# Kernel optimization log

Hardware: AMD Instinct MI355X
Metric: run time of the kernel (lower is better)

Reference implementation:

```python
import jax, jax.numpy as jnp
import numpy as np

N_SUB, N_AGR, N_URB = 100000, 200000, 100000
E_SS, E_AS, E_US = 1_600_000, 400_000, 200_000
D_SUB, D_HRU, H, OUT, L = 128, 32, 128, 16, 3


def setup_inputs() -> dict:
    key = jax.random.key(0)
    ks = jax.random.split(key, 20)
    s = 0.05
    inp = {
        "x_sub": jax.random.normal(ks[0], (N_SUB, D_SUB), jnp.float32),
        "x_agr": jax.random.normal(ks[1], (N_AGR, D_HRU), jnp.float32),
        "x_urb": jax.random.normal(ks[2], (N_URB, D_HRU), jnp.float32),
        "ss_src": jax.random.randint(ks[3], (E_SS,), 0, N_SUB, jnp.int32),
        "ss_dst": jax.random.randint(ks[4], (E_SS,), 0, N_SUB, jnp.int32),
        "as_src": jax.random.randint(ks[5], (E_AS,), 0, N_AGR, jnp.int32),
        "as_dst": jax.random.randint(ks[6], (E_AS,), 0, N_SUB, jnp.int32),
        "us_src": jax.random.randint(ks[7], (E_US,), 0, N_URB, jnp.int32),
        "us_dst": jax.random.randint(ks[8], (E_US,), 0, N_SUB, jnp.int32),
        # Stacked per-layer SAGEConv params (in_sub == hidden, so uniform shapes).
        # lin_l (neighbor path, has bias) and lin_r (root path, no bias).
        "Wl_ss": jax.random.normal(ks[9], (L, H, H), jnp.float32) * s,
        "bl_ss": jnp.zeros((L, H), jnp.float32),
        "Wr_ss": jax.random.normal(ks[10], (L, H, H), jnp.float32) * s,
        "Wl_as": jax.random.normal(ks[11], (L, D_HRU, H), jnp.float32) * s,
        "bl_as": jnp.zeros((L, H), jnp.float32),
        "Wr_as": jax.random.normal(ks[12], (L, H, H), jnp.float32) * s,
        "Wl_us": jax.random.normal(ks[13], (L, D_HRU, H), jnp.float32) * s,
        "bl_us": jnp.zeros((L, H), jnp.float32),
        "Wr_us": jax.random.normal(ks[14], (L, H, H), jnp.float32) * s,
        "Wf": jax.random.normal(ks[15], (H, OUT), jnp.float32) * s,
        "bf": jnp.zeros((OUT,), jnp.float32),
    }
    return inp


def reference(x_sub, x_agr, x_urb, ss_src, ss_dst, as_src, as_dst, us_src,
              us_dst, Wl_ss, bl_ss, Wr_ss, Wl_as, bl_as, Wr_as, Wl_us, bl_us,
              Wr_us, Wf, bf):
    # Degree of each sub node under sub->sub edges (for mean aggr, layers>0).
    deg = jax.ops.segment_sum(jnp.ones((E_SS,), x_sub.dtype), ss_dst,
                              num_segments=N_SUB)
    deg = jnp.maximum(deg, 1.0)[:, None]  # [N_SUB,1]

    h = x_sub
    for i in range(L):
        # sub -> sub: gather + scatter-add (sum at layer 0, mean afterwards)
        agg_ss = jax.ops.segment_sum(h[ss_src], ss_dst, num_segments=N_SUB)
        if i > 0:
            agg_ss = agg_ss / deg  # PyG default aggr='mean' for layers > 0
        # hru_agr -> sub and hru_urb -> sub: sum aggregation (sage_aggr='sum')
        agg_as = jax.ops.segment_sum(x_agr[as_src], as_dst, num_segments=N_SUB)
        agg_us = jax.ops.segment_sum(x_urb[us_src], us_dst, num_segments=N_SUB)
        # SAGEConv: lin_l(aggr msgs) + lin_r(x_dst); HeteroConv aggr='sum'.
        out = (agg_ss @ Wl_ss[i] + bl_ss[i] + h @ Wr_ss[i]
               + agg_as @ Wl_as[i] + bl_as[i] + h @ Wr_as[i]
               + agg_us @ Wl_us[i] + bl_us[i] + h @ Wr_us[i])
        h = jax.nn.relu(out)  # norms are Identity; dropout in eval mode
    logits = h @ Wf + bf
    return jax.nn.softmax(logits, axis=1)
```

## Files before the change

kernel.cpp:

```cpp
#include <hip/hip_runtime.h>
#include <hip/hip_bf16.h>

#define N_SUB 100000
#define N_AGR 200000
#define N_URB 100000
#define E_SS  1600000
#define E_AS  400000
#define E_US  200000
#define HID   128
#define DHRU  32
#define NOUT  16
#define NL    3
#define SCAN_T 12500

typedef unsigned short u16;
typedef unsigned int u32;
typedef short bf16x8 __attribute__((ext_vector_type(8)));
typedef float f32x4 __attribute__((ext_vector_type(4)));

static __device__ __forceinline__ u16 f2b(float f) {
    u32 x = __float_as_uint(f);
    u32 r = (x + 0x7fffu + ((x >> 16) & 1u)) >> 16;
    return (u16)r;
}
static __device__ __forceinline__ float blo(u32 u) { return __uint_as_float(u << 16); }
static __device__ __forceinline__ float bhi(u32 u) { return __uint_as_float(u & 0xffff0000u); }


__global__ void hist_kernel(const int* __restrict__ dst, int* __restrict__ deg, int n) {
    int i = blockIdx.x * 256 + threadIdx.x;
    if (i < n) atomicAdd(&deg[dst[i]], 1);
}

__global__ void scan_p1(const int* __restrict__ deg, int* __restrict__ tsum) {
    int i = blockIdx.x * 256 + threadIdx.x;
    if (i >= SCAN_T) return;
    const int4* p = (const int4*)(deg + i * 8);
    int4 a = p[0], b = p[1];
    tsum[i] = a.x + a.y + a.z + a.w + b.x + b.y + b.z + b.w;
}

__global__ void scan_p2(int* __restrict__ tsum) {
    __shared__ int sh[256];
    const int tid = threadIdx.x;
    const int start = tid * 49;
    const int end = min(start + 49, SCAN_T);
    int s = 0;
    for (int i = start; i < end; ++i) s += tsum[i];
    sh[tid] = s;
    __syncthreads();
    for (int o = 1; o < 256; o <<= 1) {
        int t = (tid >= o) ? sh[tid - o] : 0;
        __syncthreads();
        sh[tid] += t;
        __syncthreads();
    }
    int off = (tid > 0) ? sh[tid - 1] : 0;
    for (int i = start; i < end; ++i) {
        int v = tsum[i];
        tsum[i] = off;
        off += v;
    }
}

__global__ void scan_p3(int* __restrict__ degcur, const int* __restrict__ tsum,
                        int* __restrict__ ro, float* __restrict__ inv_deg) {
    int i = blockIdx.x * 256 + threadIdx.x;
    if (i >= SCAN_T) return;
    int off = tsum[i];
#pragma unroll
    for (int j = 0; j < 8; ++j) {
        int idx = i * 8 + j;
        int d = degcur[idx];
        ro[idx] = off;
        inv_deg[idx] = 1.0f / (float)(d > 1 ? d : 1);
        degcur[idx] = off;
        off += d;
    }
    if (i == SCAN_T - 1) ro[N_SUB] = off;
}

__global__ void fill_kernel(const int* __restrict__ src, const int* __restrict__ dst,
                            int* __restrict__ cursor, int* __restrict__ csr, int n) {
    int i = blockIdx.x * 256 + threadIdx.x;
    if (i < n) {
        int p = atomicAdd(&cursor[dst[i]], 1);
        csr[p] = src[i];
    }
}

__global__ void scatter32_kernel(const float* __restrict__ x, const int* __restrict__ src,
                                 const int* __restrict__ dst, float* __restrict__ agg2,
                                 int nE, int off) {
    int t = blockIdx.x * 256 + threadIdx.x;
    int e = t >> 3, j = t & 7;
    if (e >= nE) return;
    int s = src[e], d = dst[e];
    const float4 v = *(const float4*)(x + (size_t)s * 32 + j * 4);
    float* p = agg2 + (size_t)d * 64 + off + j * 4;
    atomicAdd(p + 0, v.x);
    atomicAdd(p + 1, v.y);
    atomicAdd(p + 2, v.z);
    atomicAdd(p + 3, v.w);
}

__global__ void add3_kernel(const float* __restrict__ a, const float* __restrict__ b,
                            const float* __restrict__ c, float* __restrict__ o, int n) {
    int i = blockIdx.x * 256 + threadIdx.x;
    if (i < n) o[i] = a[i] + b[i] + c[i];
}

__global__ void build_bp(const float* __restrict__ Wl_ss, const float* __restrict__ Wr_ss,
                         const float* __restrict__ Wr_as, const float* __restrict__ Wr_us,
                         const float* __restrict__ Wl_as, const float* __restrict__ Wl_us,
                         u16* __restrict__ Bp) {
    int b = blockIdx.x;
    int lane = threadIdx.x;
    int lay = b / 80, rem = b % 80, s = rem / 8, c = rem % 8;
    int col = c * 16 + (lane & 15);
    u16* o = Bp + (size_t)(((lay * 80) + s * 8 + c) * 64 + lane) * 8;
#pragma unroll
    for (int j = 0; j < 8; ++j) {
        int k = s * 32 + (lane >> 4) * 8 + j;
        float v;
        if (k < 128) {
            v = Wl_ss[((size_t)lay * 128 + k) * 128 + col];
        } else if (k < 256) {
            size_t idx = ((size_t)lay * 128 + (k - 128)) * 128 + col;
            v = Wr_ss[idx] + Wr_as[idx] + Wr_us[idx];
        } else if (k < 288) {
            v = Wl_as[((size_t)lay * 32 + (k - 256)) * 128 + col];
        } else {
            v = Wl_us[((size_t)lay * 32 + (k - 288)) * 128 + col];
        }
        o[j] = f2b(v);
    }
}

__global__ void cvt_f32_bf16(const float* __restrict__ in, u16* __restrict__ o, int n4) {
    int i = blockIdx.x * 256 + threadIdx.x;
    if (i >= n4) return;
    float4 v = ((const float4*)in)[i];
    ushort4 u;
    u.x = f2b(v.x); u.y = f2b(v.y); u.z = f2b(v.z); u.w = f2b(v.w);
    ((ushort4*)o)[i] = u;
}

__global__ __launch_bounds__(256)
void agg_ss_bf16(const u32* __restrict__ h32, const int* __restrict__ ro,
                 const int* __restrict__ csr, const float* __restrict__ inv_deg,
                 u32* __restrict__ out32, int n, int use_mean) {
    int node = blockIdx.x * 4 + (threadIdx.x >> 6);
    int lane = threadIdx.x & 63;
    if (node >= n) return;
    int beg = ro[node], end = ro[node + 1];
    float a0 = 0.f, a1 = 0.f;
    int p = beg;
    for (; p + 1 < end; p += 2) {
        int s0 = csr[p], s1 = csr[p + 1];
        u32 u0 = h32[(size_t)s0 * 64 + lane];
        u32 u1 = h32[(size_t)s1 * 64 + lane];
        a0 += blo(u0) + blo(u1);
        a1 += bhi(u0) + bhi(u1);
    }
    if (p < end) {
        u32 u0 = h32[(size_t)csr[p] * 64 + lane];
        a0 += blo(u0);
        a1 += bhi(u0);
    }
    if (use_mean) {
        float iv = inv_deg[node];
        a0 *= iv; a1 *= iv;
    }
    out32[(size_t)node * 64 + lane] = (u32)f2b(a0) | ((u32)f2b(a1) << 16);
}

__global__ __launch_bounds__(256)
void layer_gemm_mfma(const u16* __restrict__ agss, const u16* __restrict__ h,
                     const float* __restrict__ agg2, const u16* __restrict__ Bp,
                     const float* __restrict__ bsum, u16* __restrict__ out, int n) {
    __shared__ __align__(16) u16 tile[4][32][136];
    const int tid = threadIdx.x;
    const int w = tid >> 6, l = tid & 63;
    const int lr = l & 15, lq = l >> 4;
    const int rows0 = blockIdx.x * 128 + w * 32;

    f32x4 acc[2][8];
#pragma unroll
    for (int rf = 0; rf < 2; ++rf)
#pragma unroll
        for (int c = 0; c < 8; ++c) acc[rf][c] = (f32x4){0.f, 0.f, 0.f, 0.f};

    const bf16x8 zf = {0, 0, 0, 0, 0, 0, 0, 0};

#pragma unroll
    for (int s = 0; s < 10; ++s) {
        bf16x8 a[2];
        if (s < 8) {
            const u16* X = (s < 4) ? agss : h;
            int koff = (s & 3) * 32 + lq * 8;
#pragma unroll
            for (int rf = 0; rf < 2; ++rf) {
                int row = rows0 + rf * 16 + lr;
                a[rf] = (row < n) ? *(const bf16x8*)(X + (size_t)row * 128 + koff) : zf;
            }
        } else {
            int koff = (s - 8) * 32 + lq * 8;
#pragma unroll
            for (int rf = 0; rf < 2; ++rf) {
                int row = rows0 + rf * 16 + lr;
                if (row < n) {
                    float4 f0 = *(const float4*)(agg2 + (size_t)row * 64 + koff);
                    float4 f1 = *(const float4*)(agg2 + (size_t)row * 64 + koff + 4);
                    bf16x8 v;
                    v[0] = (short)f2b(f0.x); v[1] = (short)f2b(f0.y);
                    v[2] = (short)f2b(f0.z); v[3] = (short)f2b(f0.w);
                    v[4] = (short)f2b(f1.x); v[5] = (short)f2b(f1.y);
                    v[6] = (short)f2b(f1.z); v[7] = (short)f2b(f1.w);
                    a[rf] = v;
                } else {
                    a[rf] = zf;
                }
            }
        }
        const u16* bp = Bp + ((size_t)(s * 8) * 64 + l) * 8;
#pragma unroll
        for (int c = 0; c < 8; ++c) {
            bf16x8 b = *(const bf16x8*)(bp + (size_t)c * 64 * 8);
            acc[0][c] = __builtin_amdgcn_mfma_f32_16x16x32_bf16(a[0], b, acc[0][c], 0, 0, 0);
            acc[1][c] = __builtin_amdgcn_mfma_f32_16x16x32_bf16(a[1], b, acc[1][c], 0, 0, 0);
        }
    }

    float bias[8];
#pragma unroll
    for (int c = 0; c < 8; ++c) bias[c] = bsum[c * 16 + lr];

#pragma unroll
    for (int rf = 0; rf < 2; ++rf)
#pragma unroll
        for (int c = 0; c < 8; ++c)
#pragma unroll
            for (int r = 0; r < 4; ++r) {
                float v = fmaxf(acc[rf][c][r] + bias[c], 0.f);
                tile[w][rf * 16 + lq * 4 + r][c * 16 + lr] = f2b(v);
            }

#pragma unroll
    for (int i = 0; i < 8; ++i) {
        int row = i * 4 + lq;
        int grow = rows0 + row;
        if (grow < n)
            *(bf16x8*)(out + (size_t)grow * 128 + lr * 8) =
                *(const bf16x8*)&tile[w][row][lr * 8];
    }
}

__global__ __launch_bounds__(256)
void final_kernel(const u32* __restrict__ h32, const float* __restrict__ Wf,
                  const float* __restrict__ bfv, float* __restrict__ out, int n) {
    __shared__ float wsh[HID * NOUT + NOUT];
    for (int i = threadIdx.x; i < HID * NOUT; i += 256) wsh[i] = Wf[i];
    if (threadIdx.x < NOUT) wsh[HID * NOUT + threadIdx.x] = bfv[threadIdx.x];
    __syncthreads();
    int t = blockIdx.x * 256 + threadIdx.x;
    int node = t >> 4, c = t & 15;
    if (node >= n) return;
    const u32* hr = h32 + (size_t)node * 64;
    float acc = wsh[HID * NOUT + c];
#pragma unroll 4
    for (int k2 = 0; k2 < 64; ++k2) {
        u32 u = hr[k2];
        acc += blo(u) * wsh[(2 * k2) * NOUT + c] + bhi(u) * wsh[(2 * k2 + 1) * NOUT + c];
    }
    float m = acc;
#pragma unroll
    for (int o = 8; o >= 1; o >>= 1) m = fmaxf(m, __shfl_xor(m, o, 16));
    float e = expf(acc - m);
    float ssum = e;
#pragma unroll
    for (int o = 8; o >= 1; o >>= 1) ssum += __shfl_xor(ssum, o, 16);
    out[(size_t)node * NOUT + c] = e / ssum;
}

extern "C" void kernel_launch(void* const* d_in, const int* in_sizes, int n_in,
                              void* d_out, int out_size, void* d_ws, size_t ws_size,
                              hipStream_t stream) {
    const float* x_sub = (const float*)d_in[0];
    const float* x_agr = (const float*)d_in[1];
    const float* x_urb = (const float*)d_in[2];
    const int* ss_src = (const int*)d_in[3];
    const int* ss_dst = (const int*)d_in[4];
    const int* as_src = (const int*)d_in[5];
    const int* as_dst = (const int*)d_in[6];
    const int* us_src = (const int*)d_in[7];
    const int* us_dst = (const int*)d_in[8];
    const float* Wl_ss = (const float*)d_in[9];
    const float* bl_ss = (const float*)d_in[10];
    const float* Wr_ss = (const float*)d_in[11];
    const float* Wl_as = (const float*)d_in[12];
    const float* bl_as = (const float*)d_in[13];
    const float* Wr_as = (const float*)d_in[14];
    const float* Wl_us = (const float*)d_in[15];
    const float* bl_us = (const float*)d_in[16];
    const float* Wr_us = (const float*)d_in[17];
    const float* Wf = (const float*)d_in[18];
    const float* bfv = (const float*)d_in[19];
    float* out = (float*)d_out;

    char* ws = (char*)d_ws;
    u16* h0      = (u16*)(ws + 0);
    u16* hA      = (u16*)(ws + 25600000);
    u16* hB      = (u16*)(ws + 51200000);
    u16* agss    = (u16*)(ws + 76800000);
    float* agg2f = (float*)(ws + 102400000);
    float* inv_deg = (float*)(ws + 128000000);
    int* ro      = (int*)(ws + 128400000);
    int* degcur  = (int*)(ws + 128800016);
    int* csr     = (int*)(ws + 129200016);
    int* tsum    = (int*)(ws + 129200016);
    u16* Bp      = (u16*)(ws + 135600016);
    float* b_sum = (float*)(ws + 135845776);

    hipMemsetAsync(degcur, 0, N_SUB * sizeof(int), stream);
    hist_kernel<<<(E_SS + 255) / 256, 256, 0, stream>>>(ss_dst, degcur, E_SS);
    scan_p1<<<(SCAN_T + 255) / 256, 256, 0, stream>>>(degcur, tsum);
    scan_p2<<<1, 256, 0, stream>>>(tsum);
    scan_p3<<<(SCAN_T + 255) / 256, 256, 0, stream>>>(degcur, tsum, ro, inv_deg);
    fill_kernel<<<(E_SS + 255) / 256, 256, 0, stream>>>(ss_src, ss_dst, degcur, csr, E_SS);

    hipMemsetAsync(agg2f, 0, (size_t)N_SUB * 64 * sizeof(float), stream);
    scatter32_kernel<<<(E_AS * 8 + 255) / 256, 256, 0, stream>>>(x_agr, as_src, as_dst, agg2f, E_AS, 0);
    scatter32_kernel<<<(E_US * 8 + 255) / 256, 256, 0, stream>>>(x_urb, us_src, us_dst, agg2f, E_US, 32);

    build_bp<<<240, 64, 0, stream>>>(Wl_ss, Wr_ss, Wr_as, Wr_us, Wl_as, Wl_us, Bp);
    add3_kernel<<<2, 256, 0, stream>>>(bl_ss, bl_as, bl_us, b_sum, NL * HID);

    cvt_f32_bf16<<<(N_SUB * HID / 4 + 255) / 256, 256, 0, stream>>>(x_sub, h0, N_SUB * HID / 4);

    const int agg_grid = (N_SUB + 3) / 4;
    const int gemm_grid = (N_SUB + 127) / 128;
    const size_t BPL = 40960;

    agg_ss_bf16<<<agg_grid, 256, 0, stream>>>((const u32*)h0, ro, csr, inv_deg, (u32*)agss, N_SUB, 0);
    layer_gemm_mfma<<<gemm_grid, 256, 0, stream>>>(agss, h0, agg2f, Bp + 0 * BPL, b_sum + 0 * HID, hA, N_SUB);

    agg_ss_bf16<<<agg_grid, 256, 0, stream>>>((const u32*)hA, ro, csr, inv_deg, (u32*)agss, N_SUB, 1);
    layer_gemm_mfma<<<gemm_grid, 256, 0, stream>>>(agss, hA, agg2f, Bp + 1 * BPL, b_sum + 1 * HID, hB, N_SUB);

    agg_ss_bf16<<<agg_grid, 256, 0, stream>>>((const u32*)hB, ro, csr, inv_deg, (u32*)agss, N_SUB, 1);
    layer_gemm_mfma<<<gemm_grid, 256, 0, stream>>>(agss, hB, agg2f, Bp + 2 * BPL, b_sum + 2 * HID, hA, N_SUB);

    final_kernel<<<(N_SUB * NOUT + 255) / 256, 256, 0, stream>>>((const u32*)hA, Wf, bfv, out, N_SUB);
}
```

Before: 930.4 us.

## Replace atomic HRU scatter with CSR gather and store bf16 aggregates

The agr->sub and urb->sub aggregations no longer scatter with float atomics. The code now builds CSR structures for both edge sets (histogram, scan, fill) and runs a per-node gather kernel that writes the summed result directly as bf16. The GEMM kernel then reads these bf16 aggregates like its other inputs instead of converting fp32 on every layer. This removes 2.4M float atomics, the 25.6MB memset and the per-layer fp32 reads, at the cost of extra histogram, scan and fill launches and atomics on the cursor arrays.

After: 798.4 us. -14.2%, faster.

```diff
diff --git a/kernel.cpp b/kernel.cpp
--- a/kernel.cpp
+++ b/kernel.cpp
@@ -64,7 +64,7 @@
 }
 
 __global__ void scan_p3(int* __restrict__ degcur, const int* __restrict__ tsum,
-                        int* __restrict__ ro, float* __restrict__ inv_deg) {
+                        int* __restrict__ ro, float* inv_deg) {
     int i = blockIdx.x * 256 + threadIdx.x;
     if (i >= SCAN_T) return;
     int off = tsum[i];
@@ -73,7 +73,7 @@
         int idx = i * 8 + j;
         int d = degcur[idx];
         ro[idx] = off;
-        inv_deg[idx] = 1.0f / (float)(d > 1 ? d : 1);
+        if (inv_deg) inv_deg[idx] = 1.0f / (float)(d > 1 ? d : 1);
         degcur[idx] = off;
         off += d;
     }
@@ -89,19 +89,25 @@
     }
 }
 
-__global__ void scatter32_kernel(const float* __restrict__ x, const int* __restrict__ src,
-                                 const int* __restrict__ dst, float* __restrict__ agg2,
-                                 int nE, int off) {
-    int t = blockIdx.x * 256 + threadIdx.x;
-    int e = t >> 3, j = t & 7;
-    if (e >= nE) return;
-    int s = src[e], d = dst[e];
-    const float4 v = *(const float4*)(x + (size_t)s * 32 + j * 4);
-    float* p = agg2 + (size_t)d * 64 + off + j * 4;
-    atomicAdd(p + 0, v.x);
-    atomicAdd(p + 1, v.y);
-    atomicAdd(p + 2, v.z);
-    atomicAdd(p + 3, v.w);
+__global__ __launch_bounds__(256)
+void agg2_gather(const float* __restrict__ x_agr, const float* __restrict__ x_urb,
+                 const int* __restrict__ ro_as, const int* __restrict__ csr_as,
+                 const int* __restrict__ ro_us, const int* __restrict__ csr_us,
+                 u16* __restrict__ agg2b, int n) {
+    int node = blockIdx.x * 4 + (threadIdx.x >> 6);
+    int lane = threadIdx.x & 63;
+    if (node >= n) return;
+    const bool is_us = lane >= 32;
+    const int col = lane & 31;
+    const int* ro = is_us ? ro_us : ro_as;
+    const int* csr = is_us ? csr_us : csr_as;
+    const float* x = is_us ? x_urb : x_agr;
+    int beg = ro[node], end = ro[node + 1];
+    float acc = 0.f;
+    for (int p = beg; p < end; ++p) {
+        acc += x[(size_t)csr[p] * 32 + col];
+    }
+    agg2b[(size_t)node * 64 + lane] = f2b(acc);
 }
 
 __global__ void add3_kernel(const float* __restrict__ a, const float* __restrict__ b,
@@ -177,7 +183,7 @@
 
 __global__ __launch_bounds__(256)
 void layer_gemm_mfma(const u16* __restrict__ agss, const u16* __restrict__ h,
-                     const float* __restrict__ agg2, const u16* __restrict__ Bp,
+                     const u16* __restrict__ agg2b, const u16* __restrict__ Bp,
                      const float* __restrict__ bsum, u16* __restrict__ out, int n) {
     __shared__ __align__(16) u16 tile[4][32][136];
     const int tid = threadIdx.x;
@@ -195,33 +201,16 @@
 
 #pragma unroll
     for (int s = 0; s < 10; ++s) {
+        const u16* X;
+        int ld, koff;
+        if (s < 4)      { X = agss;  ld = 128; koff = s * 32 + lq * 8; }
+        else if (s < 8) { X = h;     ld = 128; koff = (s - 4) * 32 + lq * 8; }
+        else            { X = agg2b; ld = 64;  koff = (s - 8) * 32 + lq * 8; }
         bf16x8 a[2];
-        if (s < 8) {
-            const u16* X = (s < 4) ? agss : h;
-            int koff = (s & 3) * 32 + lq * 8;
-#pragma unroll
-            for (int rf = 0; rf < 2; ++rf) {
-                int row = rows0 + rf * 16 + lr;
-                a[rf] = (row < n) ? *(const bf16x8*)(X + (size_t)row * 128 + koff) : zf;
-            }
-        } else {
-            int koff = (s - 8) * 32 + lq * 8;
-#pragma unroll
-            for (int rf = 0; rf < 2; ++rf) {
-                int row = rows0 + rf * 16 + lr;
-                if (row < n) {
-                    float4 f0 = *(const float4*)(agg2 + (size_t)row * 64 + koff);
-                    float4 f1 = *(const float4*)(agg2 + (size_t)row * 64 + koff + 4);
-                    bf16x8 v;
-                    v[0] = (short)f2b(f0.x); v[1] = (short)f2b(f0.y);
-                    v[2] = (short)f2b(f0.z); v[3] = (short)f2b(f0.w);
-                    v[4] = (short)f2b(f1.x); v[5] = (short)f2b(f1.y);
-                    v[6] = (short)f2b(f1.z); v[7] = (short)f2b(f1.w);
-                    a[rf] = v;
-                } else {
-                    a[rf] = zf;
-                }
-            }
+#pragma unroll
+        for (int rf = 0; rf < 2; ++rf) {
+            int row = rows0 + rf * 16 + lr;
+            a[rf] = (row < n) ? *(const bf16x8*)(X + (size_t)row * ld + koff) : zf;
         }
         const u16* bp = Bp + ((size_t)(s * 8) * 64 + l) * 8;
 #pragma unroll
@@ -313,25 +302,43 @@
     u16* hA      = (u16*)(ws + 25600000);
     u16* hB      = (u16*)(ws + 51200000);
     u16* agss    = (u16*)(ws + 76800000);
-    float* agg2f = (float*)(ws + 102400000);
-    float* inv_deg = (float*)(ws + 128000000);
-    int* ro      = (int*)(ws + 128400000);
-    int* degcur  = (int*)(ws + 128800016);
-    int* csr     = (int*)(ws + 129200016);
-    int* tsum    = (int*)(ws + 129200016);
-    u16* Bp      = (u16*)(ws + 135600016);
-    float* b_sum = (float*)(ws + 135845776);
-
-    hipMemsetAsync(degcur, 0, N_SUB * sizeof(int), stream);
-    hist_kernel<<<(E_SS + 255) / 256, 256, 0, stream>>>(ss_dst, degcur, E_SS);
-    scan_p1<<<(SCAN_T + 255) / 256, 256, 0, stream>>>(degcur, tsum);
+    u16* agg2b   = (u16*)(ws + 102400000);
+    float* inv_deg = (float*)(ws + 115200000);
+    int* ro_ss   = (int*)(ws + 115600000);
+    int* ro_as   = (int*)(ws + 116000016);
+    int* ro_us   = (int*)(ws + 116400032);
+    int* deg_ss  = (int*)(ws + 116800048);
+    int* deg_as  = (int*)(ws + 117200048);
+    int* deg_us  = (int*)(ws + 117600048);
+    int* csr_ss  = (int*)(ws + 118000048);
+    int* csr_as  = (int*)(ws + 124400048);
+    int* csr_us  = (int*)(ws + 126000048);
+    int* tsum    = (int*)(ws + 126800048);
+    u16* Bp      = (u16*)(ws + 126850048);
+    float* b_sum = (float*)(ws + 127095808);
+
+    hipMemsetAsync(deg_ss, 0, 3 * N_SUB * sizeof(int), stream);
+    hist_kernel<<<(E_SS + 255) / 256, 256, 0, stream>>>(ss_dst, deg_ss, E_SS);
+    hist_kernel<<<(E_AS + 255) / 256, 256, 0, stream>>>(as_dst, deg_as, E_AS);
+    hist_kernel<<<(E_US + 255) / 256, 256, 0, stream>>>(us_dst, deg_us, E_US);
+
+    const int scan_grid = (SCAN_T + 255) / 256;
+    scan_p1<<<scan_grid, 256, 0, stream>>>(deg_ss, tsum);
     scan_p2<<<1, 256, 0, stream>>>(tsum);
-    scan_p3<<<(SCAN_T + 255) / 256, 256, 0, stream>>>(degcur, tsum, ro, inv_deg);
-    fill_kernel<<<(E_SS + 255) / 256, 256, 0, stream>>>(ss_src, ss_dst, degcur, csr, E_SS);
-
-    hipMemsetAsync(agg2f, 0, (size_t)N_SUB * 64 * sizeof(float), stream);
-    scatter32_kernel<<<(E_AS * 8 + 255) / 256, 256, 0, stream>>>(x_agr, as_src, as_dst, agg2f, E_AS, 0);
-    scatter32_kernel<<<(E_US * 8 + 255) / 256, 256, 0, stream>>>(x_urb, us_src, us_dst, agg2f, E_US, 32);
+    scan_p3<<<scan_grid, 256, 0, stream>>>(deg_ss, tsum, ro_ss, inv_deg);
+    scan_p1<<<scan_grid, 256, 0, stream>>>(deg_as, tsum);
+    scan_p2<<<1, 256, 0, stream>>>(tsum);
+    scan_p3<<<scan_grid, 256, 0, stream>>>(deg_as, tsum, ro_as, nullptr);
+    scan_p1<<<scan_grid, 256, 0, stream>>>(deg_us, tsum);
+    scan_p2<<<1, 256, 0, stream>>>(tsum);
+    scan_p3<<<scan_grid, 256, 0, stream>>>(deg_us, tsum, ro_us, nullptr);
+
+    fill_kernel<<<(E_SS + 255) / 256, 256, 0, stream>>>(ss_src, ss_dst, deg_ss, csr_ss, E_SS);
+    fill_kernel<<<(E_AS + 255) / 256, 256, 0, stream>>>(as_src, as_dst, deg_as, csr_as, E_AS);
+    fill_kernel<<<(E_US + 255) / 256, 256, 0, stream>>>(us_src, us_dst, deg_us, csr_us, E_US);
+
+    agg2_gather<<<(N_SUB + 3) / 4, 256, 0, stream>>>(x_agr, x_urb, ro_as, csr_as,
+                                                     ro_us, csr_us, agg2b, N_SUB);
 
     build_bp<<<240, 64, 0, stream>>>(Wl_ss, Wr_ss, Wr_as, Wr_us, Wl_as, Wl_us, Bp);
     add3_kernel<<<2, 256, 0, stream>>>(bl_ss, bl_as, bl_us, b_sum, NL * HID);
@@ -342,14 +349,14 @@
     const int gemm_grid = (N_SUB + 127) / 128;
     const size_t BPL = 40960;
 
-    agg_ss_bf16<<<agg_grid, 256, 0, stream>>>((const u32*)h0, ro, csr, inv_deg, (u32*)agss, N_SUB, 0);
-    layer_gemm_mfma<<<gemm_grid, 256, 0, stream>>>(agss, h0, agg2f, Bp + 0 * BPL, b_sum + 0 * HID, hA, N_SUB);
-
-    agg_ss_bf16<<<agg_grid, 256, 0, stream>>>((const u32*)hA, ro, csr, inv_deg, (u32*)agss, N_SUB, 1);
-    layer_gemm_mfma<<<gemm_grid, 256, 0, stream>>>(agss, hA, agg2f, Bp + 1 * BPL, b_sum + 1 * HID, hB, N_SUB);
-
-    agg_ss_bf16<<<agg_grid, 256, 0, stream>>>((const u32*)hB, ro, csr, inv_deg, (u32*)agss, N_SUB, 1);
-    layer_gemm_mfma<<<gemm_grid, 256, 0, stream>>>(agss, hB, agg2f, Bp + 2 * BPL, b_sum + 2 * HID, hA, N_SUB);
+    agg_ss_bf16<<<agg_grid, 256, 0, stream>>>((const u32*)h0, ro_ss, csr_ss, inv_deg, (u32*)agss, N_SUB, 0);
+    layer_gemm_mfma<<<gemm_grid, 256, 0, stream>>>(agss, h0, agg2b, Bp + 0 * BPL, b_sum + 0 * HID, hA, N_SUB);
+
+    agg_ss_bf16<<<agg_grid, 256, 0, stream>>>((const u32*)hA, ro_ss, csr_ss, inv_deg, (u32*)agss, N_SUB, 1);
+    layer_gemm_mfma<<<gemm_grid, 256, 0, stream>>>(agss, hA, agg2b, Bp + 1 * BPL, b_sum + 1 * HID, hB, N_SUB);
+
+    agg_ss_bf16<<<agg_grid, 256, 0, stream>>>((const u32*)hB, ro_ss, csr_ss, inv_deg, (u32*)agss, N_SUB, 1);
+    layer_gemm_mfma<<<gemm_grid, 256, 0, stream>>>(agss, hB, agg2b, Bp + 2 * BPL, b_sum + 2 * HID, hA, N_SUB);
 
     final_kernel<<<(N_SUB * NOUT + 255) / 256, 256, 0, stream>>>((const u32*)hA, Wf, bfv, out, N_SUB);
 }
```
